# Performance work log

Hardware: AMD Instinct MI355X
Metric: run time of the kernel (lower is better)

The kernel has to match this reference:

```python
import jax, jax.numpy as jnp
import numpy as np

B, L, D = 1, 2048, 2048
NH, NKV, HD = 32, 8, 64          # heads, kv heads, head_dim = D // NH
THETA = 50000.0
EPS = 1e-5
SCALE = HD ** -0.5


def _rope(x):
    # traditional (interleaved-pair) RoPE; x: (B, H, L, HD)
    hd = x.shape[-1]
    pos = jnp.arange(x.shape[2], dtype=jnp.float32)
    inv = THETA ** (-jnp.arange(0, hd, 2, dtype=jnp.float32) / hd)
    ang = pos[:, None] * inv[None, :]              # (L, HD/2)
    cos, sin = jnp.cos(ang), jnp.sin(ang)
    x1, x2 = x[..., ::2], x[..., 1::2]
    r1 = x1 * cos - x2 * sin
    r2 = x1 * sin + x2 * cos
    return jnp.stack([r1, r2], axis=-1).reshape(x.shape)


def _rmsnorm(x, w):
    return x * jax.lax.rsqrt(jnp.mean(x * x, axis=-1, keepdims=True) + EPS) * w


def setup_inputs() -> dict:
    key = jax.random.key(0)
    ks = jax.random.split(key, 5)
    x = jax.random.normal(ks[0], (B, L, D), dtype=jnp.float32)
    w_qkv = jax.random.normal(ks[1], (NH * HD + 2 * NKV * HD, D), dtype=jnp.float32) * 0.02
    w_out = jax.random.normal(ks[2], (D, D), dtype=jnp.float32) * 0.02
    q_gamma = 1.0 + 0.02 * jax.random.normal(ks[3], (HD,), dtype=jnp.float32)
    k_gamma = 1.0 + 0.02 * jax.random.normal(ks[4], (HD,), dtype=jnp.float32)
    mask = jnp.tril(jnp.ones((L, L), dtype=bool))   # causal
    return {"x": x, "w_qkv": w_qkv, "w_out": w_out,
            "q_gamma": q_gamma, "k_gamma": k_gamma, "mask": mask}


def reference(x, w_qkv, w_out, q_gamma, k_gamma, mask):
    b, l, d = x.shape
    qkv = x @ w_qkv.T                               # fused QKV proj (no bias)
    q, k, v = jnp.split(qkv, [NH * HD, NH * HD + NKV * HD], axis=-1)
    q = q.reshape(b, l, NH, HD).transpose(0, 2, 1, 3)     # (B,NH,L,HD)
    k = k.reshape(b, l, NKV, HD).transpose(0, 2, 1, 3)    # (B,NKV,L,HD)
    v = v.reshape(b, l, NKV, HD).transpose(0, 2, 1, 3)
    q = _rmsnorm(_rope(q), q_gamma)
    k = _rmsnorm(_rope(k), k_gamma)
    g = NH // NKV                                   # GQA group size
    qg = q.reshape(b, NKV, g, l, HD)
    scores = jnp.einsum('bkgqd,bkld->bkgql', qg, k) * SCALE
    scores = jnp.where(mask, scores, -jnp.inf)
    attn = jax.nn.softmax(scores, axis=-1)
    out = jnp.einsum('bkgql,bkld->bkgqd', attn, v)  # (B,NKV,g,L,HD)
    out = out.reshape(b, NH, l, HD).transpose(0, 2, 1, 3).reshape(b, l, d)
    return out @ w_out.T
```

## Files before the change

### kernel.cpp

```cpp
#include <hip/hip_runtime.h>

using bf16   = __bf16;
using bf16x4 = __bf16 __attribute__((ext_vector_type(4)));
using bf16x8 = __bf16 __attribute__((ext_vector_type(8)));
using f32x4  = float __attribute__((ext_vector_type(4)));
using f32x16 = float __attribute__((ext_vector_type(16)));
using u32x2  = unsigned int __attribute__((ext_vector_type(2)));
using u32x4  = unsigned int __attribute__((ext_vector_type(4)));

#define L_SEQ  2048
#define DMODEL 2048
#define NQH    32
#define NKVH   8
#define HDIM   64
#define QKV_N  3072

#define KVF_HSTRIDE (64 * 4 * 64 * 8)

__device__ __forceinline__ void gload_lds16(const void* g, void* lds) {
  __builtin_amdgcn_global_load_lds((__attribute__((address_space(1))) void*)(g),
                                   (__attribute__((address_space(3))) void*)(lds),
                                   16, 0, 0);
}

__device__ __forceinline__ unsigned pack2(float a, float b) {
  union { bf16 h[2]; unsigned u; } x;
  x.h[0] = (bf16)a; x.h[1] = (bf16)b;
  return x.u;
}

__global__ void cvt_f32_bf16(const float* __restrict__ in, bf16* __restrict__ out, long n) {
  const long stride = (long)gridDim.x * blockDim.x;
  const long n4 = n >> 2;
  for (long i = (long)blockIdx.x * blockDim.x + threadIdx.x; i < n4; i += stride) {
    const float4 v = reinterpret_cast<const float4*>(in)[i];
    bf16x4 o = { (bf16)v.x, (bf16)v.y, (bf16)v.z, (bf16)v.w };
    reinterpret_cast<bf16x4*>(out)[i] = o;
  }
}

template <typename OutT>
__global__ __launch_bounds__(128)
void gemm_bt(const bf16* __restrict__ A, const bf16* __restrict__ B,
             OutT* __restrict__ C, int M, int N, int K) {
  __shared__ bf16 As[128 * 64];
  __shared__ bf16 Bs[64 * 64];
  const int tid = threadIdx.x;
  const int w = tid >> 6, l = tid & 63;
  const int lq = l & 15, lg = l >> 4;
  const long m0 = (long)blockIdx.y * 128;
  const long n0 = (long)blockIdx.x * 64;

  const int lrow = l >> 3;
  const int scol = ((l & 7) ^ lrow) << 3;

  f32x4 acc[4][4];
#pragma unroll
  for (int i = 0; i < 4; ++i)
#pragma unroll
    for (int j = 0; j < 4; ++j) acc[i][j] = f32x4{0.f, 0.f, 0.f, 0.f};

  for (int k0 = 0; k0 < K; k0 += 64) {
#pragma unroll
    for (int i = 0; i < 8; ++i) {
      const int r0 = (i * 2 + w) * 8;
      gload_lds16(A + (m0 + r0 + lrow) * (long)K + k0 + scol, &As[r0 * 64]);
    }
#pragma unroll
    for (int i = 0; i < 4; ++i) {
      const int r0 = (i * 2 + w) * 8;
      gload_lds16(B + (n0 + r0 + lrow) * (long)K + k0 + scol, &Bs[r0 * 64]);
    }
    __syncthreads();
#pragma unroll
    for (int kk = 0; kk < 2; ++kk) {
      bf16x8 af[4], bfr[4];
#pragma unroll
      for (int t = 0; t < 4; ++t) {
        const int rowA = w * 64 + t * 16 + lq;
        const int blkA = (kk * 4 + lg) ^ (rowA & 7);
        af[t] = *reinterpret_cast<const bf16x8*>(&As[rowA * 64 + blkA * 8]);
        const int rowB = t * 16 + lq;
        const int blkB = (kk * 4 + lg) ^ (rowB & 7);
        bfr[t] = *reinterpret_cast<const bf16x8*>(&Bs[rowB * 64 + blkB * 8]);
      }
#pragma unroll
      for (int mt = 0; mt < 4; ++mt)
#pragma unroll
        for (int nt = 0; nt < 4; ++nt)
          acc[mt][nt] = __builtin_amdgcn_mfma_f32_16x16x32_bf16(af[mt], bfr[nt], acc[mt][nt], 0, 0, 0);
    }
    __syncthreads();
  }

#pragma unroll
  for (int mt = 0; mt < 4; ++mt)
#pragma unroll
    for (int r = 0; r < 4; ++r) {
      const long row = m0 + w * 64 + mt * 16 + lg * 4 + r;
#pragma unroll
      for (int nt = 0; nt < 4; ++nt) {
        const long col = n0 + nt * 16 + lq;
        C[row * (long)N + col] = (OutT)acc[mt][nt][r];
      }
    }
}

__global__ __launch_bounds__(256)
void rope_rms(const bf16* __restrict__ qkv, const float* __restrict__ qg,
              const float* __restrict__ kg, bf16* __restrict__ qo, bf16* __restrict__ kfr) {
  const int gid = blockIdx.x * 4 + (threadIdx.x >> 6);
  const int lane = threadIdx.x & 63;
  const int pos = gid / 40;
  const int hh = gid % 40;
  const bool isq = hh < 32;
  const int col = isq ? hh * HDIM : NQH * HDIM + (hh - 32) * HDIM;

  float x = (float)qkv[(long)pos * QKV_N + col + lane];
  float p = __shfl_xor(x, 1);
  const float fi = (float)(lane & ~1) * (1.0f / 64.0f);
  const float inv = powf(50000.0f, -fi);
  const float ang = (float)pos * inv;
  const float sn = sinf(ang), cs = cosf(ang);
  const float r = (lane & 1) ? (p * sn + x * cs) : (x * cs - p * sn);

  float ss = r * r;
#pragma unroll
  for (int off = 1; off < 64; off <<= 1) ss += __shfl_xor(ss, off);
  const float scl = rsqrtf(ss * (1.0f / 64.0f) + 1e-5f);
  const float g = isq ? qg[lane] : kg[lane];
  const float o = r * scl * g;

  if (isq) {
    qo[(long)pos * DMODEL + hh * HDIM + lane] = (bf16)(o * 0.18033688011112042f);
  } else {
    const int kvh = hh - 32;
    const int d = lane;
    const int lp = (pos & 31) + (((d >> 3) & 1) << 5);
    const long idx = ((((long)kvh * 64 + (pos >> 5)) * 4 + (d >> 4)) * 64 + lp) * 8 + (d & 7);
    kfr[idx] = (bf16)o;
  }
}

__global__ __launch_bounds__(256)
void repack_v(const bf16* __restrict__ qkv, bf16* __restrict__ vfr) {
  __shared__ bf16 t[32][72];
  const int kvh = blockIdx.x >> 6;
  const int kb = blockIdx.x & 63;
  const int tid = threadIdx.x;

  {
    const int row = tid >> 3;
    const int cc = (tid & 7) * 8;
    const bf16* g = qkv + (long)(kb * 32 + row) * QKV_N + (NQH * HDIM + NKVH * HDIM) + kvh * HDIM + cc;
    *reinterpret_cast<u32x4*>(&t[row][cc]) = *reinterpret_cast<const u32x4*>(g);
  }
  __syncthreads();

  const int f = tid >> 6, l = tid & 63;
  const int s = f >> 1, dh = f & 1;
  const int hi = l >> 5, l31 = l & 31;
  union { bf16 b[8]; u32x4 u; } o;
#pragma unroll
  for (int e = 0; e < 8; ++e) o.b[e] = t[s * 16 + hi * 8 + e][dh * 32 + l31];
  bf16* od = vfr + (((long)(kvh * 64 + kb) * 4 + f) * 64 + l) * 8;
  *reinterpret_cast<u32x4*>(od) = o.u;
}

__global__ __launch_bounds__(256)
void flash_attn(const bf16* __restrict__ Q, const bf16* __restrict__ Kfr,
                const bf16* __restrict__ Vfr, bf16* __restrict__ Og) {
  const int w = threadIdx.x >> 6, l = threadIdx.x & 63;
  const int lane31 = l & 31, hi = l >> 5;
  const int wg = blockIdx.x * 4 + w;
  const int h = wg & 31;
  const int qi = 63 - (wg >> 5);
  const int kvh = h >> 2;
  const int q0 = qi * 32;
  const int q_abs = q0 + lane31;
  const int l8 = l * 8;

  const bf16* qrow = Q + (long)q_abs * DMODEL + h * HDIM + hi * 8;
  bf16x8 qf[4];
#pragma unroll
  for (int c = 0; c < 4; ++c) qf[c] = *reinterpret_cast<const bf16x8*>(qrow + c * 16);

  f32x16 o0, o1;
#pragma unroll
  for (int r = 0; r < 16; ++r) { o0[r] = 0.f; o1[r] = 0.f; }
  float m = -3.0e38f, lsum = 0.f;

  const bf16* kfrh = Kfr + (long)kvh * KVF_HSTRIDE;
  const bf16* vfrh = Vfr + (long)kvh * KVF_HSTRIDE;

  const int nst = qi + 1;

  bf16x8 kc0, kc1, kc2, kc3;
  {
    const bf16* kp = kfrh + l8;
    kc0 = *reinterpret_cast<const bf16x8*>(kp);
    kc1 = *reinterpret_cast<const bf16x8*>(kp + 512);
    kc2 = *reinterpret_cast<const bf16x8*>(kp + 1024);
    kc3 = *reinterpret_cast<const bf16x8*>(kp + 1536);
  }

  for (int sti = 0; sti < nst; ++sti) {
    const int kb0 = sti * 32;

    const bf16* vp = vfrh + (long)sti * 2048 + l8;
    const bf16x8 va0 = *reinterpret_cast<const bf16x8*>(vp);
    const bf16x8 vb0 = *reinterpret_cast<const bf16x8*>(vp + 512);
    const bf16x8 va1 = *reinterpret_cast<const bf16x8*>(vp + 1024);
    const bf16x8 vb1 = *reinterpret_cast<const bf16x8*>(vp + 1536);

    const long knoff = (sti + 1 < nst) ? (long)(sti + 1) * 2048 : 0;
    const bf16* kp = kfrh + knoff + l8;
    const bf16x8 kn0 = *reinterpret_cast<const bf16x8*>(kp);
    const bf16x8 kn1 = *reinterpret_cast<const bf16x8*>(kp + 512);
    const bf16x8 kn2 = *reinterpret_cast<const bf16x8*>(kp + 1024);
    const bf16x8 kn3 = *reinterpret_cast<const bf16x8*>(kp + 1536);

    f32x16 st;
#pragma unroll
    for (int r = 0; r < 16; ++r) st[r] = 0.f;
    __builtin_amdgcn_s_setprio(1);
    st = __builtin_amdgcn_mfma_f32_32x32x16_bf16(kc0, qf[0], st, 0, 0, 0);
    st = __builtin_amdgcn_mfma_f32_32x32x16_bf16(kc1, qf[1], st, 0, 0, 0);
    st = __builtin_amdgcn_mfma_f32_32x32x16_bf16(kc2, qf[2], st, 0, 0, 0);
    st = __builtin_amdgcn_mfma_f32_32x32x16_bf16(kc3, qf[3], st, 0, 0, 0);
    __builtin_amdgcn_s_setprio(0);

    if (kb0 + 31 > q0) {
#pragma unroll
      for (int r = 0; r < 16; ++r) {
        const int k_abs = kb0 + (r & 3) + 8 * (r >> 2) + 4 * hi;
        if (k_abs > q_abs) st[r] = -3.0e38f;
      }
    }

    float mx = st[0];
#pragma unroll
    for (int r = 1; r < 16; ++r) mx = fmaxf(mx, st[r]);
    mx = fmaxf(mx, __shfl_xor(mx, 32));
    if (!__all(mx - m <= 8.0f)) {
      const float mn = fmaxf(m, mx);
      const float al = __builtin_amdgcn_exp2f(m - mn);
      m = mn; lsum *= al;
#pragma unroll
      for (int r = 0; r < 16; ++r) { o0[r] *= al; o1[r] *= al; }
    }
    float p[16];
    float rs = 0.f;
#pragma unroll
    for (int r = 0; r < 16; ++r) { p[r] = __builtin_amdgcn_exp2f(st[r] - m); rs += p[r]; }
    rs += __shfl_xor(rs, 32);
    lsum += rs;

#pragma unroll
    for (int s = 0; s < 2; ++s) {
      const int j = s * 8;
      const unsigned W0 = pack2(p[j + 0], p[j + 1]);
      const unsigned W1 = pack2(p[j + 2], p[j + 3]);
      const unsigned W2 = pack2(p[j + 4], p[j + 5]);
      const unsigned W3 = pack2(p[j + 6], p[j + 7]);
      u32x4 pw;
#if __has_builtin(__builtin_amdgcn_permlane32_swap)
      {
        using i32x2 = int __attribute__((ext_vector_type(2)));
        const i32x2 r02 = __builtin_amdgcn_permlane32_swap((int)W0, (int)W2, false, false);
        const i32x2 r13 = __builtin_amdgcn_permlane32_swap((int)W1, (int)W3, false, false);
        pw = u32x4{ (unsigned)r02[0], (unsigned)r13[0], (unsigned)r02[1], (unsigned)r13[1] };
      }
#else
      {
        const unsigned X0 = (unsigned)__shfl_xor((int)W0, 32);
        const unsigned X1 = (unsigned)__shfl_xor((int)W1, 32);
        const unsigned X2 = (unsigned)__shfl_xor((int)W2, 32);
        const unsigned X3 = (unsigned)__shfl_xor((int)W3, 32);
        pw = u32x4{ hi ? X2 : W0, hi ? X3 : W1, hi ? W2 : X0, hi ? W3 : X1 };
      }
#endif
      const bf16x8 pf = __builtin_bit_cast(bf16x8, pw);
      __builtin_amdgcn_s_setprio(1);
      if (s == 0) {
        o0 = __builtin_amdgcn_mfma_f32_32x32x16_bf16(va0, pf, o0, 0, 0, 0);
        o1 = __builtin_amdgcn_mfma_f32_32x32x16_bf16(vb0, pf, o1, 0, 0, 0);
      } else {
        o0 = __builtin_amdgcn_mfma_f32_32x32x16_bf16(va1, pf, o0, 0, 0, 0);
        o1 = __builtin_amdgcn_mfma_f32_32x32x16_bf16(vb1, pf, o1, 0, 0, 0);
      }
      __builtin_amdgcn_s_setprio(0);
    }

    kc0 = kn0; kc1 = kn1; kc2 = kn2; kc3 = kn3;
  }

  const float rl = 1.0f / lsum;
  bf16* orow = Og + (long)q_abs * DMODEL + h * HDIM;
#pragma unroll
  for (int g = 0; g < 4; ++g) {
    const int d0 = 8 * g + 4 * hi;
    u32x2 s0 = { pack2(o0[4 * g + 0] * rl, o0[4 * g + 1] * rl),
                 pack2(o0[4 * g + 2] * rl, o0[4 * g + 3] * rl) };
    u32x2 s1 = { pack2(o1[4 * g + 0] * rl, o1[4 * g + 1] * rl),
                 pack2(o1[4 * g + 2] * rl, o1[4 * g + 3] * rl) };
    *reinterpret_cast<u32x2*>(orow + d0) = s0;
    *reinterpret_cast<u32x2*>(orow + 32 + d0) = s1;
  }
}

extern "C" void kernel_launch(void* const* d_in, const int* in_sizes, int n_in,
                              void* d_out, int out_size, void* d_ws, size_t ws_size,
                              hipStream_t stream) {
  const float* x       = (const float*)d_in[0];
  const float* w_qkv   = (const float*)d_in[1];
  const float* w_out   = (const float*)d_in[2];
  const float* q_gamma = (const float*)d_in[3];
  const float* k_gamma = (const float*)d_in[4];

  char* ws = (char*)d_ws;
  bf16* xb  = (bf16*)(ws);
  bf16* wqb = (bf16*)(ws + (8ul  << 20));
  bf16* wob = (bf16*)(ws + (20ul << 20));
  bf16* qkv = (bf16*)(ws + (28ul << 20));
  bf16* qb  = (bf16*)(ws + (40ul << 20));
  bf16* kfr = (bf16*)(ws + (48ul << 20));
  bf16* vfr = (bf16*)(ws + (50ul << 20));
  bf16* ao  = (bf16*)(ws + (52ul << 20));
  float* out = (float*)d_out;

  cvt_f32_bf16<<<2048, 256, 0, stream>>>(x, xb, (long)L_SEQ * DMODEL);
  cvt_f32_bf16<<<2048, 256, 0, stream>>>(w_qkv, wqb, (long)QKV_N * DMODEL);
  cvt_f32_bf16<<<2048, 256, 0, stream>>>(w_out, wob, (long)DMODEL * DMODEL);

  gemm_bt<bf16><<<dim3(QKV_N / 64, L_SEQ / 128), 128, 0, stream>>>(xb, wqb, qkv, L_SEQ, QKV_N, DMODEL);

  rope_rms<<<(L_SEQ * 40) / 4, 256, 0, stream>>>(qkv, q_gamma, k_gamma, qb, kfr);
  repack_v<<<NKVH * (L_SEQ / 32), 256, 0, stream>>>(qkv, vfr);

  flash_attn<<<(NQH * (L_SEQ / 32)) / 4, 256, 0, stream>>>(qb, kfr, vfr, ao);

  gemm_bt<float><<<dim3(DMODEL / 64, L_SEQ / 128), 128, 0, stream>>>(ao, wob, out, L_SEQ, DMODEL, DMODEL);
}
```

Before: 171.7 us.

## Split KV range for long causal query tiles and merge partials in combine kernel

Query tiles in the second half of the sequence now process their causal KV range in two halves, each in a separate wave. Each half writes unnormalised fp32 partial outputs plus row max and sum to workspace, and a new combine kernel merges them with log-sum-exp rescaling. Work is paired across the four waves of a block so each block gets similar total work, and the grid grows from 512 to 768 blocks. The aim is to fix causal load imbalance and raise parallelism, at the cost of an extra launch, fp32 partial traffic through memory, and dropping the s_setprio hints around the MFMAs.

```diff
diff --git a/kernel.cpp b/kernel.cpp
--- a/kernel.cpp
+++ b/kernel.cpp
@@ -169,12 +169,35 @@
 
 __global__ __launch_bounds__(256)
 void flash_attn(const bf16* __restrict__ Q, const bf16* __restrict__ Kfr,
-                const bf16* __restrict__ Vfr, bf16* __restrict__ Og) {
+                const bf16* __restrict__ Vfr, bf16* __restrict__ Og,
+                float* __restrict__ po, float* __restrict__ pm, float* __restrict__ pl) {
   const int w = threadIdx.x >> 6, l = threadIdx.x & 63;
   const int lane31 = l & 31, hi = l >> 5;
-  const int wg = blockIdx.x * 4 + w;
-  const int h = wg & 31;
-  const int qi = 63 - (wg >> 5);
+  const int bb = blockIdx.x;
+
+  int h, qi, s0, s1, part;
+  bool split;
+  if (bb < 512) {
+    h = bb & 31;
+    const int a = bb >> 5;
+    const int xs[4] = { a, 31 - a, 32 + a, 63 - a };
+    const int x = xs[w];
+    qi = 63 - (x >> 1);
+    part = x & 1;
+    const int nst = qi + 1, h1 = (nst + 1) >> 1;
+    s0 = part ? h1 : 0;
+    s1 = part ? nst : h1;
+    split = true;
+  } else {
+    const int u = bb - 512;
+    h = u & 31;
+    const int b = u >> 5;
+    const int ys[4] = { b, 15 - b, 16 + b, 31 - b };
+    qi = 31 - ys[w];
+    s0 = 0; s1 = qi + 1; part = 0;
+    split = false;
+  }
+
   const int kvh = h >> 2;
   const int q0 = qi * 32;
   const int q_abs = q0 + lane31;
@@ -193,18 +216,16 @@
   const bf16* kfrh = Kfr + (long)kvh * KVF_HSTRIDE;
   const bf16* vfrh = Vfr + (long)kvh * KVF_HSTRIDE;
 
-  const int nst = qi + 1;
-
   bf16x8 kc0, kc1, kc2, kc3;
   {
-    const bf16* kp = kfrh + l8;
+    const bf16* kp = kfrh + (long)s0 * 2048 + l8;
     kc0 = *reinterpret_cast<const bf16x8*>(kp);
     kc1 = *reinterpret_cast<const bf16x8*>(kp + 512);
     kc2 = *reinterpret_cast<const bf16x8*>(kp + 1024);
     kc3 = *reinterpret_cast<const bf16x8*>(kp + 1536);
   }
 
-  for (int sti = 0; sti < nst; ++sti) {
+  for (int sti = s0; sti < s1; ++sti) {
     const int kb0 = sti * 32;
 
     const bf16* vp = vfrh + (long)sti * 2048 + l8;
@@ -213,7 +234,7 @@
     const bf16x8 va1 = *reinterpret_cast<const bf16x8*>(vp + 1024);
     const bf16x8 vb1 = *reinterpret_cast<const bf16x8*>(vp + 1536);
 
-    const long knoff = (sti + 1 < nst) ? (long)(sti + 1) * 2048 : 0;
+    const long knoff = (sti + 1 < s1) ? (long)(sti + 1) * 2048 : (long)s0 * 2048;
     const bf16* kp = kfrh + knoff + l8;
     const bf16x8 kn0 = *reinterpret_cast<const bf16x8*>(kp);
     const bf16x8 kn1 = *reinterpret_cast<const bf16x8*>(kp + 512);
@@ -223,12 +244,10 @@
     f32x16 st;
 #pragma unroll
     for (int r = 0; r < 16; ++r) st[r] = 0.f;
-    __builtin_amdgcn_s_setprio(1);
     st = __builtin_amdgcn_mfma_f32_32x32x16_bf16(kc0, qf[0], st, 0, 0, 0);
     st = __builtin_amdgcn_mfma_f32_32x32x16_bf16(kc1, qf[1], st, 0, 0, 0);
     st = __builtin_amdgcn_mfma_f32_32x32x16_bf16(kc2, qf[2], st, 0, 0, 0);
     st = __builtin_amdgcn_mfma_f32_32x32x16_bf16(kc3, qf[3], st, 0, 0, 0);
-    __builtin_amdgcn_s_setprio(0);
 
     if (kb0 + 31 > q0) {
 #pragma unroll
@@ -281,7 +300,6 @@
       }
 #endif
       const bf16x8 pf = __builtin_bit_cast(bf16x8, pw);
-      __builtin_amdgcn_s_setprio(1);
       if (s == 0) {
         o0 = __builtin_amdgcn_mfma_f32_32x32x16_bf16(va0, pf, o0, 0, 0, 0);
         o1 = __builtin_amdgcn_mfma_f32_32x32x16_bf16(vb0, pf, o1, 0, 0, 0);
@@ -289,24 +307,77 @@
         o0 = __builtin_amdgcn_mfma_f32_32x32x16_bf16(va1, pf, o0, 0, 0, 0);
         o1 = __builtin_amdgcn_mfma_f32_32x32x16_bf16(vb1, pf, o1, 0, 0, 0);
       }
-      __builtin_amdgcn_s_setprio(0);
     }
 
     kc0 = kn0; kc1 = kn1; kc2 = kn2; kc3 = kn3;
   }
 
-  const float rl = 1.0f / lsum;
-  bf16* orow = Og + (long)q_abs * DMODEL + h * HDIM;
-#pragma unroll
-  for (int g = 0; g < 4; ++g) {
-    const int d0 = 8 * g + 4 * hi;
-    u32x2 s0 = { pack2(o0[4 * g + 0] * rl, o0[4 * g + 1] * rl),
-                 pack2(o0[4 * g + 2] * rl, o0[4 * g + 3] * rl) };
-    u32x2 s1 = { pack2(o1[4 * g + 0] * rl, o1[4 * g + 1] * rl),
-                 pack2(o1[4 * g + 2] * rl, o1[4 * g + 3] * rl) };
-    *reinterpret_cast<u32x2*>(orow + d0) = s0;
-    *reinterpret_cast<u32x2*>(orow + 32 + d0) = s1;
-  }
+  if (split) {
+    const int pidx = (h * 32 + (qi - 32)) * 2 + part;
+    float* pbase = po + (long)pidx * 2048 + lane31 * 64;
+#pragma unroll
+    for (int g = 0; g < 4; ++g) {
+      const int d0 = 8 * g + 4 * hi;
+      *reinterpret_cast<f32x4*>(pbase + d0) =
+          f32x4{ o0[4 * g + 0], o0[4 * g + 1], o0[4 * g + 2], o0[4 * g + 3] };
+      *reinterpret_cast<f32x4*>(pbase + 32 + d0) =
+          f32x4{ o1[4 * g + 0], o1[4 * g + 1], o1[4 * g + 2], o1[4 * g + 3] };
+    }
+    if (hi == 0) {
+      pm[pidx * 32 + lane31] = m;
+      pl[pidx * 32 + lane31] = lsum;
+    }
+  } else {
+    const float rl = 1.0f / lsum;
+    bf16* orow = Og + (long)q_abs * DMODEL + h * HDIM;
+#pragma unroll
+    for (int g = 0; g < 4; ++g) {
+      const int d0 = 8 * g + 4 * hi;
+      u32x2 s0v = { pack2(o0[4 * g + 0] * rl, o0[4 * g + 1] * rl),
+                    pack2(o0[4 * g + 2] * rl, o0[4 * g + 3] * rl) };
+      u32x2 s1v = { pack2(o1[4 * g + 0] * rl, o1[4 * g + 1] * rl),
+                    pack2(o1[4 * g + 2] * rl, o1[4 * g + 3] * rl) };
+      *reinterpret_cast<u32x2*>(orow + d0) = s0v;
+      *reinterpret_cast<u32x2*>(orow + 32 + d0) = s1v;
+    }
+  }
+}
+
+__global__ __launch_bounds__(256)
+void combine_split(const float* __restrict__ po, const float* __restrict__ pm,
+                   const float* __restrict__ pl, bf16* __restrict__ ao) {
+  const int t = blockIdx.x * 2 + (threadIdx.x >> 7);
+  const int tid7 = threadIdx.x & 127;
+  const int r = tid7 >> 2;
+  const int dc = (tid7 & 3) * 16;
+  const int h = t >> 5, qi32 = t & 31;
+  const int pA = t * 2, pB = pA + 1;
+
+  const float ma = pm[pA * 32 + r], mb = pm[pB * 32 + r];
+  const float la = pl[pA * 32 + r], lb = pl[pB * 32 + r];
+  const float M = fmaxf(ma, mb);
+  const float ea = __builtin_amdgcn_exp2f(ma - M);
+  const float eb = __builtin_amdgcn_exp2f(mb - M);
+  const float inv = 1.0f / (la * ea + lb * eb);
+  const float fa = ea * inv, fb = eb * inv;
+
+  const float* oa = po + (long)pA * 2048 + r * 64 + dc;
+  const float* ob = po + (long)pB * 2048 + r * 64 + dc;
+  const long q_abs = (long)(qi32 + 32) * 32 + r;
+  bf16* od = ao + q_abs * DMODEL + h * HDIM + dc;
+
+  union { bf16 b[16]; u32x4 u[2]; } o;
+#pragma unroll
+  for (int j = 0; j < 4; ++j) {
+    const float4 a = reinterpret_cast<const float4*>(oa)[j];
+    const float4 b = reinterpret_cast<const float4*>(ob)[j];
+    o.b[4 * j + 0] = (bf16)(a.x * fa + b.x * fb);
+    o.b[4 * j + 1] = (bf16)(a.y * fa + b.y * fb);
+    o.b[4 * j + 2] = (bf16)(a.z * fa + b.z * fb);
+    o.b[4 * j + 3] = (bf16)(a.w * fa + b.w * fb);
+  }
+  *reinterpret_cast<u32x4*>(od) = o.u[0];
+  *reinterpret_cast<u32x4*>(od + 8) = o.u[1];
 }
 
 extern "C" void kernel_launch(void* const* d_in, const int* in_sizes, int n_in,
@@ -327,6 +398,9 @@
   bf16* kfr = (bf16*)(ws + (48ul << 20));
   bf16* vfr = (bf16*)(ws + (50ul << 20));
   bf16* ao  = (bf16*)(ws + (52ul << 20));
+  float* po = (float*)(ws);
+  float* pm = (float*)(ws + (16ul << 20));
+  float* pl = (float*)(ws + (16ul << 20) + (1ul << 18));
   float* out = (float*)d_out;
 
   cvt_f32_bf16<<<2048, 256, 0, stream>>>(x, xb, (long)L_SEQ * DMODEL);
@@ -338,7 +412,8 @@
   rope_rms<<<(L_SEQ * 40) / 4, 256, 0, stream>>>(qkv, q_gamma, k_gamma, qb, kfr);
   repack_v<<<NKVH * (L_SEQ / 32), 256, 0, stream>>>(qkv, vfr);
 
-  flash_attn<<<(NQH * (L_SEQ / 32)) / 4, 256, 0, stream>>>(qb, kfr, vfr, ao);
+  flash_attn<<<768, 256, 0, stream>>>(qb, kfr, vfr, ao, po, pm, pl);
+  combine_split<<<512, 256, 0, stream>>>(po, pm, pl, ao);
 
   gemm_bt<float><<<dim3(DMODEL / 64, L_SEQ / 128), 128, 0, stream>>>(ao, wob, out, L_SEQ, DMODEL, DMODEL);
 }
```

Result: no change. 173.7 us (+1.1%).

## Split causal attention KV range into chunks with separate combine kernel

Applied to the files above, without the earlier changes.

Flash attention now splits each query tile's KV range into up to four chunks of 16 key tiles, so the causal workload is spread more evenly across 1280 blocks. Each block also groups the four query heads that share one KV head. Partial outputs, maxima and sums are written to workspace, and a new combine kernel merges them with log-sum-exp weights. The change also drops the setprio hints and reworks the max reduction into a tree. In exchange it adds an extra kernel launch, bf16 rounding of partial outputs, and workspace traffic that reuses the already-consumed xb/qkv buffers.

```diff
diff --git a/kernel.cpp b/kernel.cpp
--- a/kernel.cpp
+++ b/kernel.cpp
@@ -27,6 +27,40 @@
   union { bf16 h[2]; unsigned u; } x;
   x.h[0] = (bf16)a; x.h[1] = (bf16)b;
   return x.u;
+}
+
+__device__ __forceinline__ bf16x8 make_pfrag(float p0, float p1, float p2, float p3,
+                                             float p4, float p5, float p6, float p7,
+                                             int hi) {
+  const unsigned W0 = pack2(p0, p1);
+  const unsigned W1 = pack2(p2, p3);
+  const unsigned W2 = pack2(p4, p5);
+  const unsigned W3 = pack2(p6, p7);
+  u32x4 pw;
+#if __has_builtin(__builtin_amdgcn_permlane32_swap)
+  {
+    using i32x2 = int __attribute__((ext_vector_type(2)));
+    const i32x2 r02 = __builtin_amdgcn_permlane32_swap((int)W0, (int)W2, false, false);
+    const i32x2 r13 = __builtin_amdgcn_permlane32_swap((int)W1, (int)W3, false, false);
+    pw = u32x4{ (unsigned)r02[0], (unsigned)r13[0], (unsigned)r02[1], (unsigned)r13[1] };
+  }
+#else
+  {
+    const unsigned X0 = (unsigned)__shfl_xor((int)W0, 32);
+    const unsigned X1 = (unsigned)__shfl_xor((int)W1, 32);
+    const unsigned X2 = (unsigned)__shfl_xor((int)W2, 32);
+    const unsigned X3 = (unsigned)__shfl_xor((int)W3, 32);
+    pw = u32x4{ hi ? X2 : W0, hi ? X3 : W1, hi ? W2 : X0, hi ? W3 : X1 };
+  }
+#endif
+  return __builtin_bit_cast(bf16x8, pw);
+}
+
+__device__ __forceinline__ int chunk_base(int qi) {
+  return (qi < 16) ? qi
+       : (qi < 32) ? 16 + 2 * (qi - 16)
+       : (qi < 48) ? 48 + 3 * (qi - 32)
+                   : 96 + 4 * (qi - 48);
 }
 
 __global__ void cvt_f32_bf16(const float* __restrict__ in, bf16* __restrict__ out, long n) {
@@ -169,13 +203,25 @@
 
 __global__ __launch_bounds__(256)
 void flash_attn(const bf16* __restrict__ Q, const bf16* __restrict__ Kfr,
-                const bf16* __restrict__ Vfr, bf16* __restrict__ Og) {
+                const bf16* __restrict__ Vfr,
+                bf16* __restrict__ po, float* __restrict__ pm, float* __restrict__ pl) {
   const int w = threadIdx.x >> 6, l = threadIdx.x & 63;
   const int lane31 = l & 31, hi = l >> 5;
-  const int wg = blockIdx.x * 4 + w;
-  const int h = wg & 31;
-  const int qi = 63 - (wg >> 5);
-  const int kvh = h >> 2;
+  const int bb = blockIdx.x;
+  const int kvh = bb & 7;
+  const int g = bb >> 3;
+
+  int qi, c;
+  if (g < 16)      { qi = g;                  c = 0; }
+  else if (g < 48) { qi = 16 + ((g - 16) >> 1); c = (g - 16) & 1; }
+  else if (g < 96) { qi = 32 + (g - 48) / 3;    c = (g - 48) % 3; }
+  else             { qi = 48 + ((g - 96) >> 2); c = (g - 96) & 3; }
+
+  const int h = kvh * 4 + w;
+  const int s0 = c * 16;
+  const int s1 = min(qi + 1, s0 + 16);
+  const int pidx = h * 160 + g;
+
   const int q0 = qi * 32;
   const int q_abs = q0 + lane31;
   const int l8 = l * 8;
@@ -183,7 +229,7 @@
   const bf16* qrow = Q + (long)q_abs * DMODEL + h * HDIM + hi * 8;
   bf16x8 qf[4];
 #pragma unroll
-  for (int c = 0; c < 4; ++c) qf[c] = *reinterpret_cast<const bf16x8*>(qrow + c * 16);
+  for (int cc = 0; cc < 4; ++cc) qf[cc] = *reinterpret_cast<const bf16x8*>(qrow + cc * 16);
 
   f32x16 o0, o1;
 #pragma unroll
@@ -193,18 +239,16 @@
   const bf16* kfrh = Kfr + (long)kvh * KVF_HSTRIDE;
   const bf16* vfrh = Vfr + (long)kvh * KVF_HSTRIDE;
 
-  const int nst = qi + 1;
-
   bf16x8 kc0, kc1, kc2, kc3;
   {
-    const bf16* kp = kfrh + l8;
+    const bf16* kp = kfrh + (long)s0 * 2048 + l8;
     kc0 = *reinterpret_cast<const bf16x8*>(kp);
     kc1 = *reinterpret_cast<const bf16x8*>(kp + 512);
     kc2 = *reinterpret_cast<const bf16x8*>(kp + 1024);
     kc3 = *reinterpret_cast<const bf16x8*>(kp + 1536);
   }
 
-  for (int sti = 0; sti < nst; ++sti) {
+  for (int sti = s0; sti < s1; ++sti) {
     const int kb0 = sti * 32;
 
     const bf16* vp = vfrh + (long)sti * 2048 + l8;
@@ -213,7 +257,7 @@
     const bf16x8 va1 = *reinterpret_cast<const bf16x8*>(vp + 1024);
     const bf16x8 vb1 = *reinterpret_cast<const bf16x8*>(vp + 1536);
 
-    const long knoff = (sti + 1 < nst) ? (long)(sti + 1) * 2048 : 0;
+    const long knoff = (sti + 1 < s1) ? (long)(sti + 1) * 2048 : (long)s0 * 2048;
     const bf16* kp = kfrh + knoff + l8;
     const bf16x8 kn0 = *reinterpret_cast<const bf16x8*>(kp);
     const bf16x8 kn1 = *reinterpret_cast<const bf16x8*>(kp + 512);
@@ -223,12 +267,10 @@
     f32x16 st;
 #pragma unroll
     for (int r = 0; r < 16; ++r) st[r] = 0.f;
-    __builtin_amdgcn_s_setprio(1);
     st = __builtin_amdgcn_mfma_f32_32x32x16_bf16(kc0, qf[0], st, 0, 0, 0);
     st = __builtin_amdgcn_mfma_f32_32x32x16_bf16(kc1, qf[1], st, 0, 0, 0);
     st = __builtin_amdgcn_mfma_f32_32x32x16_bf16(kc2, qf[2], st, 0, 0, 0);
     st = __builtin_amdgcn_mfma_f32_32x32x16_bf16(kc3, qf[3], st, 0, 0, 0);
-    __builtin_amdgcn_s_setprio(0);
 
     if (kb0 + 31 > q0) {
 #pragma unroll
@@ -238,10 +280,15 @@
       }
     }
 
-    float mx = st[0];
-#pragma unroll
-    for (int r = 1; r < 16; ++r) mx = fmaxf(mx, st[r]);
-    mx = fmaxf(mx, __shfl_xor(mx, 32));
+    float t[8];
+#pragma unroll
+    for (int r = 0; r < 8; ++r) t[r] = fmaxf(st[r], st[r + 8]);
+#pragma unroll
+    for (int s = 4; s > 0; s >>= 1)
+#pragma unroll
+      for (int r = 0; r < 4; ++r) if (r < s) t[r] = fmaxf(t[r], t[r + s]);
+    float mx = fmaxf(t[0], __shfl_xor(t[0], 32));
+
     if (!__all(mx - m <= 8.0f)) {
       const float mn = fmaxf(m, mx);
       const float al = __builtin_amdgcn_exp2f(m - mn);
@@ -249,64 +296,91 @@
 #pragma unroll
       for (int r = 0; r < 16; ++r) { o0[r] *= al; o1[r] *= al; }
     }
-    float p[16];
     float rs = 0.f;
 #pragma unroll
-    for (int r = 0; r < 16; ++r) { p[r] = __builtin_amdgcn_exp2f(st[r] - m); rs += p[r]; }
+    for (int r = 0; r < 16; ++r) { st[r] = __builtin_amdgcn_exp2f(st[r] - m); rs += st[r]; }
     rs += __shfl_xor(rs, 32);
     lsum += rs;
 
-#pragma unroll
-    for (int s = 0; s < 2; ++s) {
-      const int j = s * 8;
-      const unsigned W0 = pack2(p[j + 0], p[j + 1]);
-      const unsigned W1 = pack2(p[j + 2], p[j + 3]);
-      const unsigned W2 = pack2(p[j + 4], p[j + 5]);
-      const unsigned W3 = pack2(p[j + 6], p[j + 7]);
-      u32x4 pw;
-#if __has_builtin(__builtin_amdgcn_permlane32_swap)
-      {
-        using i32x2 = int __attribute__((ext_vector_type(2)));
-        const i32x2 r02 = __builtin_amdgcn_permlane32_swap((int)W0, (int)W2, false, false);
-        const i32x2 r13 = __builtin_amdgcn_permlane32_swap((int)W1, (int)W3, false, false);
-        pw = u32x4{ (unsigned)r02[0], (unsigned)r13[0], (unsigned)r02[1], (unsigned)r13[1] };
+    {
+      const bf16x8 pf0 = make_pfrag(st[0], st[1], st[2], st[3], st[4], st[5], st[6], st[7], hi);
+      o0 = __builtin_amdgcn_mfma_f32_32x32x16_bf16(va0, pf0, o0, 0, 0, 0);
+      o1 = __builtin_amdgcn_mfma_f32_32x32x16_bf16(vb0, pf0, o1, 0, 0, 0);
+      const bf16x8 pf1 = make_pfrag(st[8], st[9], st[10], st[11], st[12], st[13], st[14], st[15], hi);
+      o0 = __builtin_amdgcn_mfma_f32_32x32x16_bf16(va1, pf1, o0, 0, 0, 0);
+      o1 = __builtin_amdgcn_mfma_f32_32x32x16_bf16(vb1, pf1, o1, 0, 0, 0);
+    }
+
+    kc0 = kn0; kc1 = kn1; kc2 = kn2; kc3 = kn3;
+  }
+
+  bf16* pbase = po + (long)pidx * 2048 + lane31 * 64;
+#pragma unroll
+  for (int gg = 0; gg < 4; ++gg) {
+    const int d0 = 8 * gg + 4 * hi;
+    u32x2 s0v = { pack2(o0[4 * gg + 0], o0[4 * gg + 1]),
+                  pack2(o0[4 * gg + 2], o0[4 * gg + 3]) };
+    u32x2 s1v = { pack2(o1[4 * gg + 0], o1[4 * gg + 1]),
+                  pack2(o1[4 * gg + 2], o1[4 * gg + 3]) };
+    *reinterpret_cast<u32x2*>(pbase + d0) = s0v;
+    *reinterpret_cast<u32x2*>(pbase + 32 + d0) = s1v;
+  }
+  if (hi == 0) {
+    pm[pidx * 32 + lane31] = m;
+    pl[pidx * 32 + lane31] = lsum;
+  }
+}
+
+__global__ __launch_bounds__(256)
+void combine_split(const bf16* __restrict__ po, const float* __restrict__ pm,
+                   const float* __restrict__ pl, bf16* __restrict__ ao) {
+  const int t = blockIdx.x * 2 + (threadIdx.x >> 7);
+  const int tid7 = threadIdx.x & 127;
+  const int r = tid7 >> 2;
+  const int dc = (tid7 & 3) * 16;
+  const int h = t >> 6, qi = t & 63;
+  const int nc = 1 + (qi >> 4);
+  const int p0 = h * 160 + chunk_base(qi);
+
+  float mv0 = -3e38f, mv1 = -3e38f, mv2 = -3e38f, mv3 = -3e38f;
+  float lv0 = 0.f, lv1 = 0.f, lv2 = 0.f, lv3 = 0.f;
+  mv0 = pm[(p0 + 0) * 32 + r];              lv0 = pl[(p0 + 0) * 32 + r];
+  if (nc > 1) { mv1 = pm[(p0 + 1) * 32 + r]; lv1 = pl[(p0 + 1) * 32 + r]; }
+  if (nc > 2) { mv2 = pm[(p0 + 2) * 32 + r]; lv2 = pl[(p0 + 2) * 32 + r]; }
+  if (nc > 3) { mv3 = pm[(p0 + 3) * 32 + r]; lv3 = pl[(p0 + 3) * 32 + r]; }
+  const float M = fmaxf(fmaxf(mv0, mv1), fmaxf(mv2, mv3));
+  const float w0 = __builtin_amdgcn_exp2f(mv0 - M);
+  const float w1 = (nc > 1) ? __builtin_amdgcn_exp2f(mv1 - M) : 0.f;
+  const float w2 = (nc > 2) ? __builtin_amdgcn_exp2f(mv2 - M) : 0.f;
+  const float w3 = (nc > 3) ? __builtin_amdgcn_exp2f(mv3 - M) : 0.f;
+  const float invL = 1.0f / (lv0 * w0 + lv1 * w1 + lv2 * w2 + lv3 * w3);
+
+  float acc[16];
+#pragma unroll
+  for (int j = 0; j < 16; ++j) acc[j] = 0.f;
+
+#pragma unroll
+  for (int c = 0; c < 4; ++c) {
+    if (c < nc) {
+      const float fc = ((c == 0) ? w0 : (c == 1) ? w1 : (c == 2) ? w2 : w3) * invL;
+      const bf16* src = po + ((long)(p0 + c) * 2048) + r * 64 + dc;
+      const bf16x8 a0 = *reinterpret_cast<const bf16x8*>(src);
+      const bf16x8 a1 = *reinterpret_cast<const bf16x8*>(src + 8);
+#pragma unroll
+      for (int j = 0; j < 8; ++j) {
+        acc[j]     += (float)a0[j] * fc;
+        acc[8 + j] += (float)a1[j] * fc;
       }
-#else
-      {
-        const unsigned X0 = (unsigned)__shfl_xor((int)W0, 32);
-        const unsigned X1 = (unsigned)__shfl_xor((int)W1, 32);
-        const unsigned X2 = (unsigned)__shfl_xor((int)W2, 32);
-        const unsigned X3 = (unsigned)__shfl_xor((int)W3, 32);
-        pw = u32x4{ hi ? X2 : W0, hi ? X3 : W1, hi ? W2 : X0, hi ? W3 : X1 };
-      }
-#endif
-      const bf16x8 pf = __builtin_bit_cast(bf16x8, pw);
-      __builtin_amdgcn_s_setprio(1);
-      if (s == 0) {
-        o0 = __builtin_amdgcn_mfma_f32_32x32x16_bf16(va0, pf, o0, 0, 0, 0);
-        o1 = __builtin_amdgcn_mfma_f32_32x32x16_bf16(vb0, pf, o1, 0, 0, 0);
-      } else {
-        o0 = __builtin_amdgcn_mfma_f32_32x32x16_bf16(va1, pf, o0, 0, 0, 0);
-        o1 = __builtin_amdgcn_mfma_f32_32x32x16_bf16(vb1, pf, o1, 0, 0, 0);
-      }
-      __builtin_amdgcn_s_setprio(0);
-    }
-
-    kc0 = kn0; kc1 = kn1; kc2 = kn2; kc3 = kn3;
-  }
-
-  const float rl = 1.0f / lsum;
-  bf16* orow = Og + (long)q_abs * DMODEL + h * HDIM;
-#pragma unroll
-  for (int g = 0; g < 4; ++g) {
-    const int d0 = 8 * g + 4 * hi;
-    u32x2 s0 = { pack2(o0[4 * g + 0] * rl, o0[4 * g + 1] * rl),
-                 pack2(o0[4 * g + 2] * rl, o0[4 * g + 3] * rl) };
-    u32x2 s1 = { pack2(o1[4 * g + 0] * rl, o1[4 * g + 1] * rl),
-                 pack2(o1[4 * g + 2] * rl, o1[4 * g + 3] * rl) };
-    *reinterpret_cast<u32x2*>(orow + d0) = s0;
-    *reinterpret_cast<u32x2*>(orow + 32 + d0) = s1;
-  }
+    }
+  }
+
+  const long q_abs = (long)qi * 32 + r;
+  bf16* od = ao + q_abs * DMODEL + h * HDIM + dc;
+  union { bf16 b[16]; u32x4 u[2]; } o;
+#pragma unroll
+  for (int j = 0; j < 16; ++j) o.b[j] = (bf16)acc[j];
+  *reinterpret_cast<u32x4*>(od) = o.u[0];
+  *reinterpret_cast<u32x4*>(od + 8) = o.u[1];
 }
 
 extern "C" void kernel_launch(void* const* d_in, const int* in_sizes, int n_in,
@@ -327,6 +401,9 @@
   bf16* kfr = (bf16*)(ws + (48ul << 20));
   bf16* vfr = (bf16*)(ws + (50ul << 20));
   bf16* ao  = (bf16*)(ws + (52ul << 20));
+  bf16*  po = (bf16*)(ws);
+  float* pm = (float*)(ws + (28ul << 20));
+  float* pl = (float*)(ws + (29ul << 20));
   float* out = (float*)d_out;
 
   cvt_f32_bf16<<<2048, 256, 0, stream>>>(x, xb, (long)L_SEQ * DMODEL);
@@ -338,7 +415,8 @@
   rope_rms<<<(L_SEQ * 40) / 4, 256, 0, stream>>>(qkv, q_gamma, k_gamma, qb, kfr);
   repack_v<<<NKVH * (L_SEQ / 32), 256, 0, stream>>>(qkv, vfr);
 
-  flash_attn<<<(NQH * (L_SEQ / 32)) / 4, 256, 0, stream>>>(qb, kfr, vfr, ao);
+  flash_attn<<<1280, 256, 0, stream>>>(qb, kfr, vfr, po, pm, pl);
+  combine_split<<<1024, 256, 0, stream>>>(po, pm, pl, ao);
 
   gemm_bt<float><<<dim3(DMODEL / 64, L_SEQ / 128), 128, 0, stream>>>(ao, wob, out, L_SEQ, DMODEL, DMODEL);
 }
```

New measurement: 172.6 us. Within noise of the previous version (+0.5%).
